# Kernel optimization log

Measured on AMD Instinct MI355X. Metric: run time of the kernel, lower is better.

The kernel has to match this reference:

```python
import jax, jax.numpy as jnp
import numpy as np

B, S, DM, H, HD, M = 2, 1024, 1024, 16, 64, 32  # batch, seq, d_model, heads, head_dim, retrieved
EPS = 1e-5


def setup_inputs() -> dict:
    key = jax.random.key(0)
    ks = jax.random.split(key, 8)
    w = lambda k, shp: (jax.random.normal(k, shp) * 0.02).astype(jnp.float32)
    return {
        "previous_hidden": jax.random.normal(ks[0], (B, S, DM), jnp.float32),
        "mem_kv": jax.random.normal(ks[1], (B, S, M, 2, DM), jnp.float32),  # retrieved [k,v] from knn_memory.search
        "g_val": jax.random.uniform(ks[2], (1,), jnp.float32),
        "ln1_g": jnp.ones((DM,), jnp.float32), "ln1_b": jnp.zeros((DM,), jnp.float32),
        "c_attn_w": w(ks[3], (DM, 3 * DM)), "c_attn_b": jnp.zeros((3 * DM,), jnp.float32),
        "c_proj_w": w(ks[4], (DM, DM)), "c_proj_b": jnp.zeros((DM,), jnp.float32),
        "ln2_g": jnp.ones((DM,), jnp.float32), "ln2_b": jnp.zeros((DM,), jnp.float32),
        "fc_w": w(ks[5], (DM, 4 * DM)), "fc_b": jnp.zeros((4 * DM,), jnp.float32),
        "proj_w": w(ks[6], (4 * DM, DM)), "proj_b": jnp.zeros((DM,), jnp.float32),
    }


def _ln(x, g, b):
    m = jnp.mean(x, -1, keepdims=True)
    v = jnp.mean(jnp.square(x - m), -1, keepdims=True)
    return (x - m) * jax.lax.rsqrt(v + EPS) * g + b


def _split(t):  # [b,s,(h d)] -> [b,h,s,d]
    return t.reshape(B, S, H, HD).transpose(0, 2, 1, 3)


def _merge(t):  # [b,h,s,d] -> [b,s,(h d)]
    return t.transpose(0, 2, 1, 3).reshape(B, S, DM)


def _forward(previous_hidden, mem_kv, g_val, ln1_g, ln1_b, c_attn_w, c_attn_b,
             c_proj_w, c_proj_b, ln2_g, ln2_b, fc_w, fc_b, proj_w, proj_b):
    residual = previous_hidden
    h = _ln(previous_hidden, ln1_g, ln1_b)
    qkv = h @ c_attn_w + c_attn_b
    q, k, v = jnp.split(qkv, 3, axis=-1)
    q, k, v = _split(q), _split(k), _split(v)  # [b,h,s,d]

    # --- memory attention over retrieved k/v (per query position, M candidates) ---
    mem_k = mem_kv[..., 0, :].reshape(B, S, M, H, HD).transpose(0, 3, 1, 2, 4)  # [b,h,s,m,d]
    mem_v = mem_kv[..., 1, :].reshape(B, S, M, H, HD).transpose(0, 3, 1, 2, 4)
    mw = jnp.einsum('bhsd,bhsmd->bhsm', q, mem_k) / jnp.sqrt(jnp.asarray(HD, q.dtype))
    mw = jax.nn.softmax(mw, axis=-1)
    mem_attn_output = _merge(jnp.einsum('bhsm,bhsmd->bhsd', mw, mem_v))  # pre-c_proj (source overwrites c_proj'd output)

    # --- standard causal self-attention (GPT-2 block attn, incl. its c_proj) ---
    scores = jnp.einsum('bhqd,bhkd->bhqk', q, k) / jnp.sqrt(jnp.asarray(HD, q.dtype))
    causal = jnp.tril(jnp.ones((S, S), bool))
    scores = jnp.where(causal, scores, jnp.finfo(scores.dtype).min)
    p = jax.nn.softmax(scores, axis=-1)
    std_attn_output = _merge(jnp.einsum('bhqk,bhkd->bhqd', p, v)) @ c_proj_w + c_proj_b

    # gated combine (apply_linear_g=True, scalar g path since g_val.shape[0]==1)
    attn_output = (1.0 - g_val) * std_attn_output + g_val * mem_attn_output

    h = attn_output + residual
    residual2 = h
    h2 = _ln(h, ln2_g, ln2_b)
    ff = jax.nn.gelu(h2 @ fc_w + fc_b, approximate=True) @ proj_w + proj_b  # gelu_new
    return residual2 + ff


def reference(previous_hidden, mem_kv, g_val, ln1_g, ln1_b, c_attn_w, c_attn_b,
              c_proj_w, c_proj_b, ln2_g, ln2_b, fc_w, fc_b, proj_w, proj_b):
    return _forward(previous_hidden, mem_kv, g_val, ln1_g, ln1_b, c_attn_w, c_attn_b,
                    c_proj_w, c_proj_b, ln2_g, ln2_b, fc_w, fc_b, proj_w, proj_b)
```

## Files before the change

### kernel.cpp

```cpp
#include <hip/hip_runtime.h>


typedef short bf16x8 __attribute__((ext_vector_type(8)));
typedef float f32x4 __attribute__((ext_vector_type(4)));

__device__ __forceinline__ unsigned short f2b(float x) {
  unsigned int u = __float_as_uint(x);
  u += 0x7fffu + ((u >> 16) & 1u);
  return (unsigned short)(u >> 16);
}
__device__ __forceinline__ float b2f(unsigned int bits16) {
  return __uint_as_float(bits16 << 16);
}
__device__ __forceinline__ void async16(const void* g, void* l) {
  __builtin_amdgcn_global_load_lds((__attribute__((address_space(1))) void*)g,
                                   (__attribute__((address_space(3))) void*)l,
                                   16, 0, 0);
}

__global__ __launch_bounds__(256) void transpose_cast_kernel(
    const float* __restrict__ W, unsigned short* __restrict__ Wt, int K, int N) {
  __shared__ float tile[32][33];
  int n0 = blockIdx.x * 32, k0 = blockIdx.y * 32;
  int tx = threadIdx.x, ty = threadIdx.y;
#pragma unroll
  for (int i = 0; i < 4; i++)
    tile[ty + 8 * i][tx] = W[(size_t)(k0 + ty + 8 * i) * N + n0 + tx];
  __syncthreads();
#pragma unroll
  for (int i = 0; i < 4; i++)
    Wt[(size_t)(n0 + ty + 8 * i) * K + k0 + tx] = f2b(tile[tx][ty + 8 * i]);
}

__global__ __launch_bounds__(256) void ln_cast_kernel(
    const float* __restrict__ x, const float* __restrict__ gw,
    const float* __restrict__ bw, unsigned short* __restrict__ out) {
  int row = blockIdx.x, t = threadIdx.x;
  size_t base = (size_t)row * 1024 + t * 4;
  float4 v = *(const float4*)(x + base);
  float s = v.x + v.y + v.z + v.w;
  float q = v.x * v.x + v.y * v.y + v.z * v.z + v.w * v.w;
#pragma unroll
  for (int off = 32; off; off >>= 1) {
    s += __shfl_xor(s, off);
    q += __shfl_xor(q, off);
  }
  __shared__ float red[8];
  int w = t >> 6, l = t & 63;
  if (l == 0) { red[w] = s; red[w + 4] = q; }
  __syncthreads();
  s = red[0] + red[1] + red[2] + red[3];
  q = red[4] + red[5] + red[6] + red[7];
  float mean = s * (1.0f / 1024.0f);
  float var = q * (1.0f / 1024.0f) - mean * mean;
  float rstd = rsqrtf(var + 1e-5f);
  float4 g4 = *(const float4*)(gw + t * 4);
  float4 b4 = *(const float4*)(bw + t * 4);
  out[base + 0] = f2b((v.x - mean) * rstd * g4.x + b4.x);
  out[base + 1] = f2b((v.y - mean) * rstd * g4.y + b4.y);
  out[base + 2] = f2b((v.z - mean) * rstd * g4.z + b4.z);
  out[base + 3] = f2b((v.w - mean) * rstd * g4.w + b4.w);
}

template <int BM, int BN, int MODE>
__global__ __launch_bounds__(256, 2) void gemm_bf16(
    const unsigned short* __restrict__ A, const unsigned short* __restrict__ Bt,
    const float* __restrict__ bias, const float* __restrict__ res,
    void* __restrict__ outp, int N, int K) {
  constexpr int SM = BM / 32, SN = BN / 32;
  __shared__ __align__(16) unsigned short At[BM * 64];
  __shared__ __align__(16) unsigned short Bs[BN * 64];
  const int t = threadIdx.x, w = t >> 6, l = t & 63;
  const int wm = w >> 1, wn = w & 1;
  const int lq = l & 15, lk = l >> 4;
  const int m0 = blockIdx.y * BM, n0 = blockIdx.x * BN;
  const int sr = t >> 3;
  const int scs = (t & 7) ^ (sr & 7);
  const unsigned short* Ag = A + (size_t)(m0 + sr) * K + scs * 8;
  const unsigned short* Bg = Bt + (size_t)(n0 + sr) * K + scs * 8;
  unsigned short* Al = &At[(size_t)t * 8];
  unsigned short* Bl = &Bs[(size_t)t * 8];
  const int swr = (lq & 7) << 3;
  f32x4 acc[SM][SN] = {};

  for (int k0 = 0; k0 < K; k0 += 64) {
#pragma unroll
    for (int p = 0; p < BM / 32; ++p)
      async16(Ag + (size_t)(p * 32) * K + k0, Al + p * 2048);
#pragma unroll
    for (int p = 0; p < BN / 32; ++p)
      async16(Bg + (size_t)(p * 32) * K + k0, Bl + p * 2048);
    __syncthreads();
#pragma unroll
    for (int kk = 0; kk < 2; ++kk) {
      const int koff = (kk * 32 + lk * 8) ^ swr;
      bf16x8 af[SM], bv[SN];
#pragma unroll
      for (int i = 0; i < SM; i++)
        af[i] = *(const bf16x8*)&At[(wm * (BM / 2) + i * 16 + lq) * 64 + koff];
#pragma unroll
      for (int j = 0; j < SN; j++)
        bv[j] = *(const bf16x8*)&Bs[(wn * (BN / 2) + j * 16 + lq) * 64 + koff];
#pragma unroll
      for (int i = 0; i < SM; i++)
#pragma unroll
        for (int j = 0; j < SN; j++)
          acc[i][j] = __builtin_amdgcn_mfma_f32_16x16x32_bf16(af[i], bv[j], acc[i][j], 0, 0, 0);
    }
    __syncthreads();
  }

#pragma unroll
  for (int i = 0; i < SM; i++) {
    int mrow = m0 + wm * (BM / 2) + i * 16 + lk * 4;
#pragma unroll
    for (int j = 0; j < SN; j++) {
      int ncol = n0 + wn * (BN / 2) + j * 16 + lq;
      float bval = bias[ncol];
#pragma unroll
      for (int r = 0; r < 4; r++) {
        size_t idx = (size_t)(mrow + r) * N + ncol;
        float v = acc[i][j][r] + bval;
        if (MODE == 0) {
          ((unsigned short*)outp)[idx] = f2b(v);
        } else if (MODE == 1) {
          ((float*)outp)[idx] = v;
        } else if (MODE == 2) {
          float u = v + 0.044715f * v * v * v;
          float e = __expf(1.5957691216057308f * u);
          float th = 1.0f - 2.0f / (e + 1.0f);
          ((unsigned short*)outp)[idx] = f2b(0.5f * v * (1.0f + th));
        } else {
          ((float*)outp)[idx] = v + res[idx];
        }
      }
    }
  }
}

__global__ __launch_bounds__(512) void memattn_kernel(
    const unsigned short* __restrict__ qkv, const float* __restrict__ memkv,
    float* __restrict__ out) {
  int bs = blockIdx.x, t = threadIdx.x;
  __shared__ float dotb[16 * 33];
  __shared__ float wsm[512];
  int w = t >> 6, l = t & 63;
  const unsigned short* qp = qkv + (size_t)bs * 3072 + l * 16;
  bf16x8 qa = *(const bf16x8*)qp;
  bf16x8 qb = *(const bf16x8*)(qp + 8);
  float qreg[16];
#pragma unroll
  for (int i = 0; i < 8; i++) {
    qreg[i] = b2f((unsigned short)qa[i]);
    qreg[8 + i] = b2f((unsigned short)qb[i]);
  }
  const float* kbase = memkv + (size_t)bs * 65536 + (size_t)l * 16;
#pragma unroll
  for (int j = 0; j < 4; j++) {
    int m = w * 4 + j;
    const float* kp = kbase + (size_t)m * 2048;
    float dot = 0.0f;
#pragma unroll
    for (int d4 = 0; d4 < 4; d4++) {
      float4 kk = *(const float4*)(kp + d4 * 4);
      dot += kk.x * qreg[d4 * 4 + 0] + kk.y * qreg[d4 * 4 + 1] +
             kk.z * qreg[d4 * 4 + 2] + kk.w * qreg[d4 * 4 + 3];
    }
    dot += __shfl_xor(dot, 1);
    dot += __shfl_xor(dot, 2);
    if ((l & 3) == 0) dotb[(l >> 2) * 33 + m] = dot * 0.125f;
  }
  __syncthreads();
  {
    int h = t >> 5, m = t & 31;
    float d = dotb[h * 33 + m];
    float mx = d;
#pragma unroll
    for (int off = 1; off < 32; off <<= 1) mx = fmaxf(mx, __shfl_xor(mx, off));
    float e = __expf(d - mx);
    float sm = e;
#pragma unroll
    for (int off = 1; off < 32; off <<= 1) sm += __shfl_xor(sm, off);
    wsm[t] = e / sm;
  }
  __syncthreads();
  const float* vbase = memkv + (size_t)bs * 65536 + 1024;
#pragma unroll
  for (int rep = 0; rep < 2; ++rep) {
    int eidx = t + rep * 512;
    int he = eidx >> 6;
    const float* wrow = &wsm[he * 32];
    float acc = 0.0f;
#pragma unroll
    for (int mm = 0; mm < 32; ++mm) acc += wrow[mm] * vbase[(size_t)mm * 2048 + eidx];
    out[(size_t)bs * 1024 + eidx] = acc;
  }
}

__global__ __launch_bounds__(256) void flash_kernel(
    const unsigned short* __restrict__ qkv, unsigned short* __restrict__ out) {
  int blk = blockIdx.x;
  int qt = 15 - (blk & 15), bh = blk >> 4;
  int b = bh >> 4, h = bh & 15;
  int t = threadIdx.x, w = t >> 6, l = t & 63;
  int lq = l & 15, lk = l >> 4;
  __shared__ __align__(16) unsigned short Kt[32 * 72];
  __shared__ __align__(16) unsigned short Vt[64 * 40];
  __shared__ __align__(16) unsigned short Pb[4][16 * 40];

  const unsigned short* base = qkv + (size_t)b * 1024 * 3072;
  int qr0 = qt * 64 + w * 16;

  bf16x8 qf0 = *(const bf16x8*)(base + (size_t)(qr0 + lq) * 3072 + h * 64 + lk * 8);
  bf16x8 qf1 = *(const bf16x8*)(base + (size_t)(qr0 + lq) * 3072 + h * 64 + 32 + lk * 8);

  f32x4 o[4] = {};
  float mrow[4], lrow[4];
#pragma unroll
  for (int r = 0; r < 4; r++) { mrow[r] = -1e30f; lrow[r] = 0.0f; }

  int nch = (qt + 1) * 2;
  for (int c = 0; c < nch; ++c) {
    int kv0 = c * 32;
    {
      int rr = t >> 3, d8 = t & 7;
      const unsigned short* krow = base + (size_t)(kv0 + rr) * 3072 + 1024 + h * 64;
      *(bf16x8*)&Kt[rr * 72 + d8 * 8] = *(const bf16x8*)(krow + d8 * 8);
      bf16x8 v8 = *(const bf16x8*)(krow + 1024 + d8 * 8);
      int vc = rr ^ ((d8 & 3) << 3);
#pragma unroll
      for (int i = 0; i < 8; i++) Vt[(d8 * 8 + i) * 40 + vc] = (unsigned short)v8[i];
    }
    __syncthreads();

    f32x4 sv[2];
#pragma unroll
    for (int j = 0; j < 2; j++) {
      if (kv0 + j * 16 <= qr0 + 15) {
        bf16x8 k0f = *(const bf16x8*)&Kt[(j * 16 + lq) * 72 + lk * 8];
        bf16x8 k1f = *(const bf16x8*)&Kt[(j * 16 + lq) * 72 + 32 + lk * 8];
        f32x4 s = {};
        s = __builtin_amdgcn_mfma_f32_16x16x32_bf16(qf0, k0f, s, 0, 0, 0);
        s = __builtin_amdgcn_mfma_f32_16x16x32_bf16(qf1, k1f, s, 0, 0, 0);
#pragma unroll
        for (int r = 0; r < 4; r++) {
          float x = s[r] * 0.125f;
          int qrow = qr0 + lk * 4 + r;
          int kvg = kv0 + j * 16 + lq;
          if (kvg > qrow) x = -1e30f;
          s[r] = x;
        }
        sv[j] = s;
      } else {
        sv[j] = (f32x4){-1e30f, -1e30f, -1e30f, -1e30f};
      }
    }
#pragma unroll
    for (int r = 0; r < 4; r++) {
      float mnew = fmaxf(sv[0][r], sv[1][r]);
#pragma unroll
      for (int off = 1; off < 16; off <<= 1) mnew = fmaxf(mnew, __shfl_xor(mnew, off));
      mnew = fmaxf(mnew, mrow[r]);
      float a = __expf(mrow[r] - mnew);
      float e0 = __expf(sv[0][r] - mnew);
      float e1 = __expf(sv[1][r] - mnew);
      float rs = e0 + e1;
#pragma unroll
      for (int off = 1; off < 16; off <<= 1) rs += __shfl_xor(rs, off);
      lrow[r] = lrow[r] * a + rs;
      mrow[r] = mnew;
      o[0][r] *= a; o[1][r] *= a; o[2][r] *= a; o[3][r] *= a;
      Pb[w][(lk * 4 + r) * 40 + lq] = f2b(e0);
      Pb[w][(lk * 4 + r) * 40 + 16 + lq] = f2b(e1);
    }
    __syncthreads();

    if (kv0 <= qr0 + 15) {
      bf16x8 pf = *(const bf16x8*)&Pb[w][lq * 40 + lk * 8];
#pragma unroll
      for (int dt = 0; dt < 4; dt++) {
        int s = (dt * 2 + (lq >> 3)) & 3;
        bf16x8 vf = *(const bf16x8*)&Vt[(dt * 16 + lq) * 40 + ((lk ^ s) << 3)];
        o[dt] = __builtin_amdgcn_mfma_f32_16x16x32_bf16(pf, vf, o[dt], 0, 0, 0);
      }
    }
    __syncthreads();
  }

  unsigned short* op = out + (size_t)b * 1024 * 1024 + h * 64;
#pragma unroll
  for (int dt = 0; dt < 4; dt++)
#pragma unroll
    for (int r = 0; r < 4; r++) {
      float v = o[dt][r] / lrow[r];
      op[(size_t)(qr0 + lk * 4 + r) * 1024 + dt * 16 + lq] = f2b(v);
    }
}

__global__ __launch_bounds__(256) void combine_ln2_kernel(
    const float* __restrict__ stdp, const float* __restrict__ mem,
    const float* __restrict__ resid, const float* __restrict__ gval,
    const float* __restrict__ gw, const float* __restrict__ bw,
    float* __restrict__ hmid, unsigned short* __restrict__ h2) {
  int row = blockIdx.x, t = threadIdx.x;
  float g = gval[0];
  size_t base = (size_t)row * 1024 + t * 4;
  float4 a = *(const float4*)(stdp + base);
  float4 m4 = *(const float4*)(mem + base);
  float4 r4 = *(const float4*)(resid + base);
  float4 hv;
  hv.x = (1.0f - g) * a.x + g * m4.x + r4.x;
  hv.y = (1.0f - g) * a.y + g * m4.y + r4.y;
  hv.z = (1.0f - g) * a.z + g * m4.z + r4.z;
  hv.w = (1.0f - g) * a.w + g * m4.w + r4.w;
  *(float4*)(hmid + base) = hv;
  float s = hv.x + hv.y + hv.z + hv.w;
  float q = hv.x * hv.x + hv.y * hv.y + hv.z * hv.z + hv.w * hv.w;
#pragma unroll
  for (int off = 32; off; off >>= 1) {
    s += __shfl_xor(s, off);
    q += __shfl_xor(q, off);
  }
  __shared__ float red[8];
  int w = t >> 6, l = t & 63;
  if (l == 0) { red[w] = s; red[w + 4] = q; }
  __syncthreads();
  s = red[0] + red[1] + red[2] + red[3];
  q = red[4] + red[5] + red[6] + red[7];
  float mean = s * (1.0f / 1024.0f);
  float var = q * (1.0f / 1024.0f) - mean * mean;
  float rstd = rsqrtf(var + 1e-5f);
  float4 g4 = *(const float4*)(gw + t * 4);
  float4 b4 = *(const float4*)(bw + t * 4);
  h2[base + 0] = f2b((hv.x - mean) * rstd * g4.x + b4.x);
  h2[base + 1] = f2b((hv.y - mean) * rstd * g4.y + b4.y);
  h2[base + 2] = f2b((hv.z - mean) * rstd * g4.z + b4.z);
  h2[base + 3] = f2b((hv.w - mean) * rstd * g4.w + b4.w);
}

extern "C" void kernel_launch(void* const* d_in, const int* in_sizes, int n_in,
                              void* d_out, int out_size, void* d_ws, size_t ws_size,
                              hipStream_t stream) {
  const float* prev = (const float*)d_in[0];
  const float* memkv = (const float*)d_in[1];
  const float* gval = (const float*)d_in[2];
  const float* ln1g = (const float*)d_in[3];
  const float* ln1b = (const float*)d_in[4];
  const float* attw = (const float*)d_in[5];
  const float* attb = (const float*)d_in[6];
  const float* cpw = (const float*)d_in[7];
  const float* cpb = (const float*)d_in[8];
  const float* ln2g = (const float*)d_in[9];
  const float* ln2b = (const float*)d_in[10];
  const float* fcw = (const float*)d_in[11];
  const float* fcb = (const float*)d_in[12];
  const float* pjw = (const float*)d_in[13];
  const float* pjb = (const float*)d_in[14];

  char* ws = (char*)d_ws;
  size_t off = 0;
  unsigned short* wqkv_t = (unsigned short*)(ws + off); off += (size_t)3072 * 1024 * 2;
  unsigned short* wcp_t  = (unsigned short*)(ws + off); off += (size_t)1024 * 1024 * 2;
  unsigned short* wfc_t  = (unsigned short*)(ws + off); off += (size_t)4096 * 1024 * 2;
  unsigned short* wpj_t  = (unsigned short*)(ws + off); off += (size_t)1024 * 4096 * 2;
  unsigned short* h_bf   = (unsigned short*)(ws + off); off += (size_t)2048 * 1024 * 2;
  unsigned short* qkv_bf = (unsigned short*)(ws + off); off += (size_t)2048 * 3072 * 2;
  unsigned short* satt_bf= (unsigned short*)(ws + off); off += (size_t)2048 * 1024 * 2;
  unsigned short* h2_bf  = (unsigned short*)(ws + off); off += (size_t)2048 * 1024 * 2;
  float* matt  = (float*)(ws + off); off += (size_t)2048 * 1024 * 4;
  float* sproj = (float*)(ws + off); off += (size_t)2048 * 1024 * 4;
  float* hmid  = (float*)(ws + off); off += (size_t)2048 * 1024 * 4;
  unsigned short* ff1_bf = (unsigned short*)(ws + off); off += (size_t)2048 * 4096 * 2;

  dim3 tb(32, 8);
  transpose_cast_kernel<<<dim3(3072 / 32, 1024 / 32), tb, 0, stream>>>(attw, wqkv_t, 1024, 3072);
  transpose_cast_kernel<<<dim3(1024 / 32, 1024 / 32), tb, 0, stream>>>(cpw, wcp_t, 1024, 1024);
  transpose_cast_kernel<<<dim3(4096 / 32, 1024 / 32), tb, 0, stream>>>(fcw, wfc_t, 1024, 4096);
  transpose_cast_kernel<<<dim3(1024 / 32, 4096 / 32), tb, 0, stream>>>(pjw, wpj_t, 4096, 1024);

  ln_cast_kernel<<<2048, 256, 0, stream>>>(prev, ln1g, ln1b, h_bf);

  gemm_bf16<128, 128, 0><<<dim3(24, 16), 256, 0, stream>>>(h_bf, wqkv_t, attb, nullptr, qkv_bf, 3072, 1024);

  memattn_kernel<<<2048, 512, 0, stream>>>(qkv_bf, memkv, matt);
  flash_kernel<<<512, 256, 0, stream>>>(qkv_bf, satt_bf);

  gemm_bf16<128, 64, 1><<<dim3(16, 16), 256, 0, stream>>>(satt_bf, wcp_t, cpb, nullptr, sproj, 1024, 1024);

  combine_ln2_kernel<<<2048, 256, 0, stream>>>(sproj, matt, prev, gval, ln2g, ln2b, hmid, h2_bf);

  gemm_bf16<128, 128, 2><<<dim3(32, 16), 256, 0, stream>>>(h2_bf, wfc_t, fcb, nullptr, ff1_bf, 4096, 1024);

  gemm_bf16<128, 64, 3><<<dim3(16, 16), 256, 0, stream>>>(ff1_bf, wpj_t, pjb, hmid, (float*)d_out, 1024, 4096);
}
```

Before: 968.2 us.

## Double-buffer GEMM LDS tiles, fuse flash and memory attention launches, retile projections

The GEMM now double-buffers its LDS tiles, issuing the async global-to-LDS loads for the next K tile before computing the current one, so load latency overlaps with MFMA work. The flash-attention and memory-attention kernels are merged into one launch, with block IDs below 512 doing causal attention and the rest doing memory attention at 256 threads, so the two can run concurrently. The c_proj and final projection GEMMs move to 64x64 tiles with 4 waves per SIMD to get more blocks on the device. Double-buffering doubles LDS use per block, which may lower occupancy, and the memory-attention path now does more work per thread.

```diff
diff --git a/kernel.cpp b/kernel.cpp
--- a/kernel.cpp
+++ b/kernel.cpp
@@ -62,14 +62,14 @@
   out[base + 3] = f2b((v.w - mean) * rstd * g4.w + b4.w);
 }
 
-template <int BM, int BN, int MODE>
-__global__ __launch_bounds__(256, 2) void gemm_bf16(
+template <int BM, int BN, int MODE, int MINW>
+__global__ __launch_bounds__(256, MINW) void gemm_bf16(
     const unsigned short* __restrict__ A, const unsigned short* __restrict__ Bt,
     const float* __restrict__ bias, const float* __restrict__ res,
     void* __restrict__ outp, int N, int K) {
   constexpr int SM = BM / 32, SN = BN / 32;
-  __shared__ __align__(16) unsigned short At[BM * 64];
-  __shared__ __align__(16) unsigned short Bs[BN * 64];
+  __shared__ __align__(16) unsigned short At[2][BM * 64];
+  __shared__ __align__(16) unsigned short Bs[2][BN * 64];
   const int t = threadIdx.x, w = t >> 6, l = t & 63;
   const int wm = w >> 1, wn = w & 1;
   const int lq = l & 15, lk = l >> 4;
@@ -78,29 +78,35 @@
   const int scs = (t & 7) ^ (sr & 7);
   const unsigned short* Ag = A + (size_t)(m0 + sr) * K + scs * 8;
   const unsigned short* Bg = Bt + (size_t)(n0 + sr) * K + scs * 8;
-  unsigned short* Al = &At[(size_t)t * 8];
-  unsigned short* Bl = &Bs[(size_t)t * 8];
   const int swr = (lq & 7) << 3;
   f32x4 acc[SM][SN] = {};
-
-  for (int k0 = 0; k0 < K; k0 += 64) {
+  const int nt = K >> 6;
+
+  auto stage = [&](int buf, int tt) {
+    const int k0s = tt << 6;
 #pragma unroll
     for (int p = 0; p < BM / 32; ++p)
-      async16(Ag + (size_t)(p * 32) * K + k0, Al + p * 2048);
+      async16(Ag + (size_t)(p * 32) * K + k0s, &At[buf][t * 8 + p * 2048]);
 #pragma unroll
     for (int p = 0; p < BN / 32; ++p)
-      async16(Bg + (size_t)(p * 32) * K + k0, Bl + p * 2048);
-    __syncthreads();
+      async16(Bg + (size_t)(p * 32) * K + k0s, &Bs[buf][t * 8 + p * 2048]);
+  };
+
+  stage(0, 0);
+  __syncthreads();
+  int cur = 0;
+  for (int tt = 0; tt < nt; ++tt) {
+    if (tt + 1 < nt) stage(cur ^ 1, tt + 1);
 #pragma unroll
     for (int kk = 0; kk < 2; ++kk) {
       const int koff = (kk * 32 + lk * 8) ^ swr;
       bf16x8 af[SM], bv[SN];
 #pragma unroll
       for (int i = 0; i < SM; i++)
-        af[i] = *(const bf16x8*)&At[(wm * (BM / 2) + i * 16 + lq) * 64 + koff];
+        af[i] = *(const bf16x8*)&At[cur][(wm * (BM / 2) + i * 16 + lq) * 64 + koff];
 #pragma unroll
       for (int j = 0; j < SN; j++)
-        bv[j] = *(const bf16x8*)&Bs[(wn * (BN / 2) + j * 16 + lq) * 64 + koff];
+        bv[j] = *(const bf16x8*)&Bs[cur][(wn * (BN / 2) + j * 16 + lq) * 64 + koff];
 #pragma unroll
       for (int i = 0; i < SM; i++)
 #pragma unroll
@@ -108,6 +114,7 @@
           acc[i][j] = __builtin_amdgcn_mfma_f32_16x16x32_bf16(af[i], bv[j], acc[i][j], 0, 0, 0);
     }
     __syncthreads();
+    cur ^= 1;
   }
 
 #pragma unroll
@@ -138,163 +145,167 @@
   }
 }
 
-__global__ __launch_bounds__(512) void memattn_kernel(
+__global__ __launch_bounds__(256) void attn_fused_kernel(
     const unsigned short* __restrict__ qkv, const float* __restrict__ memkv,
-    float* __restrict__ out) {
-  int bs = blockIdx.x, t = threadIdx.x;
-  __shared__ float dotb[16 * 33];
-  __shared__ float wsm[512];
-  int w = t >> 6, l = t & 63;
-  const unsigned short* qp = qkv + (size_t)bs * 3072 + l * 16;
-  bf16x8 qa = *(const bf16x8*)qp;
-  bf16x8 qb = *(const bf16x8*)(qp + 8);
-  float qreg[16];
-#pragma unroll
-  for (int i = 0; i < 8; i++) {
-    qreg[i] = b2f((unsigned short)qa[i]);
-    qreg[8 + i] = b2f((unsigned short)qb[i]);
+    unsigned short* __restrict__ satt, float* __restrict__ matt) {
+  __shared__ __align__(16) unsigned short smem[7424];
+  int t = threadIdx.x;
+
+  if (blockIdx.x < 512) {
+    unsigned short* Kt = smem;
+    unsigned short* Vt = smem + 2304;
+    unsigned short* Pb = smem + 4864;
+    int blk = blockIdx.x;
+    int qt = 15 - (blk & 15), bh = blk >> 4;
+    int b = bh >> 4, h = bh & 15;
+    int w = t >> 6, l = t & 63;
+    int lq = l & 15, lk = l >> 4;
+
+    const unsigned short* base = qkv + (size_t)b * 1024 * 3072;
+    int qr0 = qt * 64 + w * 16;
+
+    bf16x8 qf0 = *(const bf16x8*)(base + (size_t)(qr0 + lq) * 3072 + h * 64 + lk * 8);
+    bf16x8 qf1 = *(const bf16x8*)(base + (size_t)(qr0 + lq) * 3072 + h * 64 + 32 + lk * 8);
+
+    f32x4 o[4] = {};
+    float mrow[4], lrow[4];
+#pragma unroll
+    for (int r = 0; r < 4; r++) { mrow[r] = -1e30f; lrow[r] = 0.0f; }
+
+    int nch = (qt + 1) * 2;
+    for (int c = 0; c < nch; ++c) {
+      int kv0 = c * 32;
+      {
+        int rr = t >> 3, d8 = t & 7;
+        const unsigned short* krow = base + (size_t)(kv0 + rr) * 3072 + 1024 + h * 64;
+        *(bf16x8*)&Kt[rr * 72 + d8 * 8] = *(const bf16x8*)(krow + d8 * 8);
+        bf16x8 v8 = *(const bf16x8*)(krow + 1024 + d8 * 8);
+        int vc = rr ^ ((d8 & 3) << 3);
+#pragma unroll
+        for (int i = 0; i < 8; i++) Vt[(d8 * 8 + i) * 40 + vc] = (unsigned short)v8[i];
+      }
+      __syncthreads();
+
+      f32x4 sv[2];
+#pragma unroll
+      for (int j = 0; j < 2; j++) {
+        if (kv0 + j * 16 <= qr0 + 15) {
+          bf16x8 k0f = *(const bf16x8*)&Kt[(j * 16 + lq) * 72 + lk * 8];
+          bf16x8 k1f = *(const bf16x8*)&Kt[(j * 16 + lq) * 72 + 32 + lk * 8];
+          f32x4 s = {};
+          s = __builtin_amdgcn_mfma_f32_16x16x32_bf16(qf0, k0f, s, 0, 0, 0);
+          s = __builtin_amdgcn_mfma_f32_16x16x32_bf16(qf1, k1f, s, 0, 0, 0);
+#pragma unroll
+          for (int r = 0; r < 4; r++) {
+            float x = s[r] * 0.125f;
+            int qrow = qr0 + lk * 4 + r;
+            int kvg = kv0 + j * 16 + lq;
+            if (kvg > qrow) x = -1e30f;
+            s[r] = x;
+          }
+          sv[j] = s;
+        } else {
+          sv[j] = (f32x4){-1e30f, -1e30f, -1e30f, -1e30f};
+        }
+      }
+#pragma unroll
+      for (int r = 0; r < 4; r++) {
+        float mnew = fmaxf(sv[0][r], sv[1][r]);
+#pragma unroll
+        for (int off = 1; off < 16; off <<= 1) mnew = fmaxf(mnew, __shfl_xor(mnew, off));
+        mnew = fmaxf(mnew, mrow[r]);
+        float a = __expf(mrow[r] - mnew);
+        float e0 = __expf(sv[0][r] - mnew);
+        float e1 = __expf(sv[1][r] - mnew);
+        float rs = e0 + e1;
+#pragma unroll
+        for (int off = 1; off < 16; off <<= 1) rs += __shfl_xor(rs, off);
+        lrow[r] = lrow[r] * a + rs;
+        mrow[r] = mnew;
+        o[0][r] *= a; o[1][r] *= a; o[2][r] *= a; o[3][r] *= a;
+        Pb[w * 640 + (lk * 4 + r) * 40 + lq] = f2b(e0);
+        Pb[w * 640 + (lk * 4 + r) * 40 + 16 + lq] = f2b(e1);
+      }
+      __syncthreads();
+
+      if (kv0 <= qr0 + 15) {
+        bf16x8 pf = *(const bf16x8*)&Pb[w * 640 + lq * 40 + lk * 8];
+#pragma unroll
+        for (int dt = 0; dt < 4; dt++) {
+          int s = (dt * 2 + (lq >> 3)) & 3;
+          bf16x8 vf = *(const bf16x8*)&Vt[(dt * 16 + lq) * 40 + ((lk ^ s) << 3)];
+          o[dt] = __builtin_amdgcn_mfma_f32_16x16x32_bf16(pf, vf, o[dt], 0, 0, 0);
+        }
+      }
+      __syncthreads();
+    }
+
+    unsigned short* op = satt + (size_t)b * 1024 * 1024 + h * 64;
+#pragma unroll
+    for (int dt = 0; dt < 4; dt++)
+#pragma unroll
+      for (int r = 0; r < 4; r++) {
+        float v = o[dt][r] / lrow[r];
+        op[(size_t)(qr0 + lk * 4 + r) * 1024 + dt * 16 + lq] = f2b(v);
+      }
+  } else {
+    float* dotb = (float*)smem;
+    float* wsm = (float*)smem + 528;
+    int bs = blockIdx.x - 512;
+    int w = t >> 6, l = t & 63;
+    const unsigned short* qp = qkv + (size_t)bs * 3072 + l * 16;
+    bf16x8 qa = *(const bf16x8*)qp;
+    bf16x8 qb = *(const bf16x8*)(qp + 8);
+    float qreg[16];
+#pragma unroll
+    for (int i = 0; i < 8; i++) {
+      qreg[i] = b2f((unsigned short)qa[i]);
+      qreg[8 + i] = b2f((unsigned short)qb[i]);
+    }
+    const float* kbase = memkv + (size_t)bs * 65536 + (size_t)l * 16;
+#pragma unroll
+    for (int j = 0; j < 8; j++) {
+      int m = w * 8 + j;
+      const float* kp = kbase + (size_t)m * 2048;
+      float dot = 0.0f;
+#pragma unroll
+      for (int d4 = 0; d4 < 4; d4++) {
+        float4 kk = *(const float4*)(kp + d4 * 4);
+        dot += kk.x * qreg[d4 * 4 + 0] + kk.y * qreg[d4 * 4 + 1] +
+               kk.z * qreg[d4 * 4 + 2] + kk.w * qreg[d4 * 4 + 3];
+      }
+      dot += __shfl_xor(dot, 1);
+      dot += __shfl_xor(dot, 2);
+      if ((l & 3) == 0) dotb[(l >> 2) * 33 + m] = dot * 0.125f;
+    }
+    __syncthreads();
+#pragma unroll
+    for (int rep = 0; rep < 2; ++rep) {
+      int idx = t + rep * 256;
+      int h = idx >> 5, m = idx & 31;
+      float d = dotb[h * 33 + m];
+      float mx = d;
+#pragma unroll
+      for (int off = 1; off < 32; off <<= 1) mx = fmaxf(mx, __shfl_xor(mx, off));
+      float e = __expf(d - mx);
+      float sm = e;
+#pragma unroll
+      for (int off = 1; off < 32; off <<= 1) sm += __shfl_xor(sm, off);
+      wsm[idx] = e / sm;
+    }
+    __syncthreads();
+    const float* vbase = memkv + (size_t)bs * 65536 + 1024;
+#pragma unroll
+    for (int rep = 0; rep < 4; ++rep) {
+      int eidx = t + rep * 256;
+      int he = eidx >> 6;
+      const float* wrow = &wsm[he * 32];
+      float acc = 0.0f;
+#pragma unroll
+      for (int mm = 0; mm < 32; ++mm) acc += wrow[mm] * vbase[(size_t)mm * 2048 + eidx];
+      matt[(size_t)bs * 1024 + eidx] = acc;
+    }
   }
-  const float* kbase = memkv + (size_t)bs * 65536 + (size_t)l * 16;
-#pragma unroll
-  for (int j = 0; j < 4; j++) {
-    int m = w * 4 + j;
-    const float* kp = kbase + (size_t)m * 2048;
-    float dot = 0.0f;
-#pragma unroll
-    for (int d4 = 0; d4 < 4; d4++) {
-      float4 kk = *(const float4*)(kp + d4 * 4);
-      dot += kk.x * qreg[d4 * 4 + 0] + kk.y * qreg[d4 * 4 + 1] +
-             kk.z * qreg[d4 * 4 + 2] + kk.w * qreg[d4 * 4 + 3];
-    }
-    dot += __shfl_xor(dot, 1);
-    dot += __shfl_xor(dot, 2);
-    if ((l & 3) == 0) dotb[(l >> 2) * 33 + m] = dot * 0.125f;
-  }
-  __syncthreads();
-  {
-    int h = t >> 5, m = t & 31;
-    float d = dotb[h * 33 + m];
-    float mx = d;
-#pragma unroll
-    for (int off = 1; off < 32; off <<= 1) mx = fmaxf(mx, __shfl_xor(mx, off));
-    float e = __expf(d - mx);
-    float sm = e;
-#pragma unroll
-    for (int off = 1; off < 32; off <<= 1) sm += __shfl_xor(sm, off);
-    wsm[t] = e / sm;
-  }
-  __syncthreads();
-  const float* vbase = memkv + (size_t)bs * 65536 + 1024;
-#pragma unroll
-  for (int rep = 0; rep < 2; ++rep) {
-    int eidx = t + rep * 512;
-    int he = eidx >> 6;
-    const float* wrow = &wsm[he * 32];
-    float acc = 0.0f;
-#pragma unroll
-    for (int mm = 0; mm < 32; ++mm) acc += wrow[mm] * vbase[(size_t)mm * 2048 + eidx];
-    out[(size_t)bs * 1024 + eidx] = acc;
-  }
-}
-
-__global__ __launch_bounds__(256) void flash_kernel(
-    const unsigned short* __restrict__ qkv, unsigned short* __restrict__ out) {
-  int blk = blockIdx.x;
-  int qt = 15 - (blk & 15), bh = blk >> 4;
-  int b = bh >> 4, h = bh & 15;
-  int t = threadIdx.x, w = t >> 6, l = t & 63;
-  int lq = l & 15, lk = l >> 4;
-  __shared__ __align__(16) unsigned short Kt[32 * 72];
-  __shared__ __align__(16) unsigned short Vt[64 * 40];
-  __shared__ __align__(16) unsigned short Pb[4][16 * 40];
-
-  const unsigned short* base = qkv + (size_t)b * 1024 * 3072;
-  int qr0 = qt * 64 + w * 16;
-
-  bf16x8 qf0 = *(const bf16x8*)(base + (size_t)(qr0 + lq) * 3072 + h * 64 + lk * 8);
-  bf16x8 qf1 = *(const bf16x8*)(base + (size_t)(qr0 + lq) * 3072 + h * 64 + 32 + lk * 8);
-
-  f32x4 o[4] = {};
-  float mrow[4], lrow[4];
-#pragma unroll
-  for (int r = 0; r < 4; r++) { mrow[r] = -1e30f; lrow[r] = 0.0f; }
-
-  int nch = (qt + 1) * 2;
-  for (int c = 0; c < nch; ++c) {
-    int kv0 = c * 32;
-    {
-      int rr = t >> 3, d8 = t & 7;
-      const unsigned short* krow = base + (size_t)(kv0 + rr) * 3072 + 1024 + h * 64;
-      *(bf16x8*)&Kt[rr * 72 + d8 * 8] = *(const bf16x8*)(krow + d8 * 8);
-      bf16x8 v8 = *(const bf16x8*)(krow + 1024 + d8 * 8);
-      int vc = rr ^ ((d8 & 3) << 3);
-#pragma unroll
-      for (int i = 0; i < 8; i++) Vt[(d8 * 8 + i) * 40 + vc] = (unsigned short)v8[i];
-    }
-    __syncthreads();
-
-    f32x4 sv[2];
-#pragma unroll
-    for (int j = 0; j < 2; j++) {
-      if (kv0 + j * 16 <= qr0 + 15) {
-        bf16x8 k0f = *(const bf16x8*)&Kt[(j * 16 + lq) * 72 + lk * 8];
-        bf16x8 k1f = *(const bf16x8*)&Kt[(j * 16 + lq) * 72 + 32 + lk * 8];
-        f32x4 s = {};
-        s = __builtin_amdgcn_mfma_f32_16x16x32_bf16(qf0, k0f, s, 0, 0, 0);
-        s = __builtin_amdgcn_mfma_f32_16x16x32_bf16(qf1, k1f, s, 0, 0, 0);
-#pragma unroll
-        for (int r = 0; r < 4; r++) {
-          float x = s[r] * 0.125f;
-          int qrow = qr0 + lk * 4 + r;
-          int kvg = kv0 + j * 16 + lq;
-          if (kvg > qrow) x = -1e30f;
-          s[r] = x;
-        }
-        sv[j] = s;
-      } else {
-        sv[j] = (f32x4){-1e30f, -1e30f, -1e30f, -1e30f};
-      }
-    }
-#pragma unroll
-    for (int r = 0; r < 4; r++) {
-      float mnew = fmaxf(sv[0][r], sv[1][r]);
-#pragma unroll
-      for (int off = 1; off < 16; off <<= 1) mnew = fmaxf(mnew, __shfl_xor(mnew, off));
-      mnew = fmaxf(mnew, mrow[r]);
-      float a = __expf(mrow[r] - mnew);
-      float e0 = __expf(sv[0][r] - mnew);
-      float e1 = __expf(sv[1][r] - mnew);
-      float rs = e0 + e1;
-#pragma unroll
-      for (int off = 1; off < 16; off <<= 1) rs += __shfl_xor(rs, off);
-      lrow[r] = lrow[r] * a + rs;
-      mrow[r] = mnew;
-      o[0][r] *= a; o[1][r] *= a; o[2][r] *= a; o[3][r] *= a;
-      Pb[w][(lk * 4 + r) * 40 + lq] = f2b(e0);
-      Pb[w][(lk * 4 + r) * 40 + 16 + lq] = f2b(e1);
-    }
-    __syncthreads();
-
-    if (kv0 <= qr0 + 15) {
-      bf16x8 pf = *(const bf16x8*)&Pb[w][lq * 40 + lk * 8];
-#pragma unroll
-      for (int dt = 0; dt < 4; dt++) {
-        int s = (dt * 2 + (lq >> 3)) & 3;
-        bf16x8 vf = *(const bf16x8*)&Vt[(dt * 16 + lq) * 40 + ((lk ^ s) << 3)];
-        o[dt] = __builtin_amdgcn_mfma_f32_16x16x32_bf16(pf, vf, o[dt], 0, 0, 0);
-      }
-    }
-    __syncthreads();
-  }
-
-  unsigned short* op = out + (size_t)b * 1024 * 1024 + h * 64;
-#pragma unroll
-  for (int dt = 0; dt < 4; dt++)
-#pragma unroll
-    for (int r = 0; r < 4; r++) {
-      float v = o[dt][r] / lrow[r];
-      op[(size_t)(qr0 + lk * 4 + r) * 1024 + dt * 16 + lq] = f2b(v);
-    }
 }
 
 __global__ __launch_bounds__(256) void combine_ln2_kernel(
@@ -380,16 +391,15 @@
 
   ln_cast_kernel<<<2048, 256, 0, stream>>>(prev, ln1g, ln1b, h_bf);
 
-  gemm_bf16<128, 128, 0><<<dim3(24, 16), 256, 0, stream>>>(h_bf, wqkv_t, attb, nullptr, qkv_bf, 3072, 1024);
-
-  memattn_kernel<<<2048, 512, 0, stream>>>(qkv_bf, memkv, matt);
-  flash_kernel<<<512, 256, 0, stream>>>(qkv_bf, satt_bf);
-
-  gemm_bf16<128, 64, 1><<<dim3(16, 16), 256, 0, stream>>>(satt_bf, wcp_t, cpb, nullptr, sproj, 1024, 1024);
+  gemm_bf16<128, 128, 0, 2><<<dim3(24, 16), 256, 0, stream>>>(h_bf, wqkv_t, attb, nullptr, qkv_bf, 3072, 1024);
+
+  attn_fused_kernel<<<2560, 256, 0, stream>>>(qkv_bf, memkv, satt_bf, matt);
+
+  gemm_bf16<64, 64, 1, 4><<<dim3(16, 32), 256, 0, stream>>>(satt_bf, wcp_t, cpb, nullptr, sproj, 1024, 1024);
 
   combine_ln2_kernel<<<2048, 256, 0, stream>>>(sproj, matt, prev, gval, ln2g, ln2b, hmid, h2_bf);
 
-  gemm_bf16<128, 128, 2><<<dim3(32, 16), 256, 0, stream>>>(h2_bf, wfc_t, fcb, nullptr, ff1_bf, 4096, 1024);
-
-  gemm_bf16<128, 64, 3><<<dim3(16, 16), 256, 0, stream>>>(ff1_bf, wpj_t, pjb, hmid, (float*)d_out, 1024, 4096);
-}
+  gemm_bf16<128, 128, 2, 2><<<dim3(32, 16), 256, 0, stream>>>(h2_bf, wfc_t, fcb, nullptr, ff1_bf, 4096, 1024);
+
+  gemm_bf16<64, 64, 3, 4><<<dim3(16, 32), 256, 0, stream>>>(ff1_bf, wpj_t, pjb, hmid, (float*)d_out, 1024, 4096);
+}
```

Measured after the change: 907.1 us. 6.3% less time.
